# Performance work log

Hardware: AMD Instinct MI355X
Metric: run time of the kernel (lower is better)

Reference implementation:

```python
import jax, jax.numpy as jnp
import numpy as np

B, S, E, H = 2, 2048, 1024, 16
DH = E // H
SCALE = DH ** -0.5

def setup_inputs() -> dict:
    key = jax.random.key(0)
    ks = jax.random.split(key, 5)
    w_std = (2.0 / (E + E)) ** 0.5  # xavier-ish scale
    return {
        'x': jax.random.normal(ks[0], (B, S, E), jnp.float32),
        'Wq': jax.random.normal(ks[1], (E, E), jnp.float32) * w_std,
        'bq': jnp.zeros((E,), jnp.float32),
        'Wk': jax.random.normal(ks[2], (E, E), jnp.float32) * w_std,
        'bk': jnp.zeros((E,), jnp.float32),
        'Wv': jax.random.normal(ks[3], (E, E), jnp.float32) * w_std,
        'bv': jnp.zeros((E,), jnp.float32),
        'Wo': jax.random.normal(ks[4], (E, E), jnp.float32) * w_std,
        'bo': jnp.zeros((E,), jnp.float32),
    }

def reference(x, Wq, bq, Wk, bk, Wv, bv, Wo, bo):
    # self-attention: query = key = value = x; torch Linear: y = x @ W.T + b
    q = (x @ Wq.T + bq) * SCALE            # [B,S,E]
    k = x @ Wk.T + bk
    v = x @ Wv.T + bv
    # split heads -> [B,S,H,DH]
    q = q.reshape(B, S, H, DH)
    k = k.reshape(B, S, H, DH)
    v = v.reshape(B, S, H, DH)
    # explicit attention matrix [B,H,S,S] (faithful to unfused bmm path)
    scores = jnp.einsum('bqhd,bkhd->bhqk', q, k)
    probs = jax.nn.softmax(scores, axis=-1)
    attn = jnp.einsum('bhqk,bkhd->bqhd', probs, v).reshape(B, S, E)
    return attn @ Wo.T + bo                # [B,S,E]
```

## Files before the change

kernel.cpp:

```cpp
#include <hip/hip_runtime.h>
#include <stdint.h>

#define BB 2
#define SS 2048
#define EE 1024
#define HH 16
#define DHD 64
#define MM (BB*SS)
#define QSCALE (0.125f * 1.4426950408889634f)

typedef __bf16 bf16;
typedef __bf16 bf16x8 __attribute__((ext_vector_type(8)));
typedef __bf16 bf16x4 __attribute__((ext_vector_type(4)));
typedef float  f32x4  __attribute__((ext_vector_type(4)));
typedef unsigned short ushort8 __attribute__((ext_vector_type(8)));

#define MFMA16(a,b,c) __builtin_amdgcn_mfma_f32_16x16x32_bf16(a,b,c,0,0,0)

__device__ __forceinline__ void gload_lds16(const void* g, void* l) {
  __builtin_amdgcn_global_load_lds(
      (const __attribute__((address_space(1))) unsigned int*)g,
      (__attribute__((address_space(3))) unsigned int*)l, 16, 0, 0);
}

__device__ __forceinline__ unsigned short f2bf(float f) {
  union { float f; unsigned u; } v; v.f = f;
  return (unsigned short)((v.u + 0x7FFFu + ((v.u >> 16) & 1u)) >> 16);
}

__global__ void convert_kernel(const float* __restrict__ x,
                               const float* __restrict__ wq, const float* __restrict__ wk,
                               const float* __restrict__ wv, const float* __restrict__ wo,
                               unsigned short* __restrict__ xbf,
                               unsigned short* __restrict__ wqb, unsigned short* __restrict__ wkb,
                               unsigned short* __restrict__ wvb, unsigned short* __restrict__ wob) {
  long t = (long)blockIdx.x * blockDim.x + threadIdx.x;
  long base = t * 8;
  const float* src; unsigned short* dst; long off;
  if (base < 4194304L) { src = x; dst = xbf; off = base; }
  else {
    long r = base - 4194304L; int j = (int)(r >> 20); off = r & 1048575L;
    src = (j==0)?wq:(j==1)?wk:(j==2)?wv:wo;
    dst = (j==0)?wqb:(j==1)?wkb:(j==2)?wvb:wob;
  }
  const float4* s4 = (const float4*)(src + off);
  float4 a = s4[0], b = s4[1];
  ushort8 o;
  o[0]=f2bf(a.x); o[1]=f2bf(a.y); o[2]=f2bf(a.z); o[3]=f2bf(a.w);
  o[4]=f2bf(b.x); o[5]=f2bf(b.y); o[6]=f2bf(b.z); o[7]=f2bf(b.w);
  *(ushort8*)(dst + off) = o;
}

#define GS_STAGE(kbuf, kt) { \
    const size_t kb_ = (size_t)(kt) * 64; \
    char* d_ = lds + (kbuf) * 16384 + tid * 16; \
    gload_lds16(a0 + kb_, d_); \
    gload_lds16(a1 + kb_, d_ + 4096); \
    gload_lds16(b0 + kb_, d_ + 8192); \
    gload_lds16(b1 + kb_, d_ + 12288); \
  }

template<bool SWAP>
__device__ __forceinline__ void gemm_kloop(
    const char* a0, const char* a1, const char* b0, const char* b1,
    char* lds, const int tid, const int (&aoff)[4], const int (&boff)[4],
    f32x4 (&acc)[4][4]) {
  GS_STAGE(0, 0);
  GS_STAGE(1, 1);
  int cur = 0;
  for (int kt = 0; kt < 32; ++kt) {
    if (kt < 31) {
      asm volatile("s_waitcnt vmcnt(4)" ::: "memory");
    } else {
      asm volatile("s_waitcnt vmcnt(0)" ::: "memory");
    }
    __builtin_amdgcn_s_barrier();
    if (kt < 30) {
      int sb = cur + 2; if (sb >= 3) sb -= 3;
      GS_STAGE(sb, kt + 2);
    }
    const char* Ts = lds + cur * 16384;
    bf16x8 af[4], bfv[4];
#pragma unroll
    for (int mt=0; mt<4; ++mt) af[mt] = *(const bf16x8*)(Ts + aoff[mt]);
#pragma unroll
    for (int nt=0; nt<4; ++nt) bfv[nt] = *(const bf16x8*)(Ts + boff[nt]);
#pragma unroll
    for (int mt=0; mt<4; ++mt)
#pragma unroll
      for (int nt=0; nt<4; ++nt)
        acc[mt][nt] = SWAP ? MFMA16(bfv[nt], af[mt], acc[mt][nt])
                           : MFMA16(af[mt], bfv[nt], acc[mt][nt]);
    cur = (cur == 2) ? 0 : cur + 1;
  }
}

__global__ __launch_bounds__(256) void qkv_gemm(
    const bf16* __restrict__ xbf,
    const bf16* __restrict__ wqb, const bf16* __restrict__ wkb, const bf16* __restrict__ wvb,
    const float* __restrict__ bq, const float* __restrict__ bk, const float* __restrict__ bv,
    bf16* __restrict__ Q, bf16* __restrict__ K, bf16* __restrict__ VT) {
  __shared__ char lds[49152] __attribute__((aligned(16)));
  const int tid = threadIdx.x;
  const int bm = blockIdx.y * 128;
  const int bnG = blockIdx.x * 128;
  const int proj = bnG >> 10;
  const int bn = bnG & 1023;
  const bf16* wsel = (proj==0)?wqb:(proj==1)?wkb:wvb;
  const float* bias = (proj==0)?bq:(proj==1)?bk:bv;

  const int lane = tid & 63, w = tid >> 6;
  const int wm = (w>>1)*64, wn = (w&1)*64;
  const int c = lane & 15, g = lane >> 4;

  const int sr = tid >> 2;
  const int scb = ((tid & 3) * 16) ^ ((sr & 3) << 4);
  const char* a0 = (const char*)xbf  + ((size_t)(bm + sr     ) * 1024) * 2 + scb;
  const char* a1 = (const char*)xbf  + ((size_t)(bm + 64 + sr) * 1024) * 2 + scb;
  const char* b0 = (const char*)wsel + ((size_t)(bn + sr     ) * 1024) * 2 + scb;
  const char* b1 = (const char*)wsel + ((size_t)(bn + 64 + sr) * 1024) * 2 + scb;

  int aoff[4], boff[4];
#pragma unroll
  for (int mt=0; mt<4; ++mt) { int rr = wm + mt*16 + c; aoff[mt] = rr*64 + ((g*16) ^ ((rr&3)<<4)); }
#pragma unroll
  for (int nt=0; nt<4; ++nt) { int rr = wn + nt*16 + c; boff[nt] = 8192 + rr*64 + ((g*16) ^ ((rr&3)<<4)); }

  f32x4 acc[4][4];
#pragma unroll
  for (int mt=0; mt<4; ++mt)
#pragma unroll
    for (int nt=0; nt<4; ++nt) acc[mt][nt] = (f32x4){0.f,0.f,0.f,0.f};

  const int bidx = bm >> 11;
  const int srow = bm & 2047;

  if (proj != 2) {
    gemm_kloop<true>(a0, a1, b0, b1, lds, tid, aoff, boff, acc);
    bf16* dst = (proj == 0) ? Q : K;
    const float qs = (proj == 0) ? QSCALE : 1.0f;
#pragma unroll
    for (int nt=0; nt<4; ++nt) {
      const int n0 = bn + wn + nt*16 + g*4;
      const float4 b4 = *(const float4*)(bias + n0);
      const int h = n0 >> 6, d0 = n0 & 63;
#pragma unroll
      for (int mt=0; mt<4; ++mt) {
        const int s = srow + wm + mt*16 + c;
        bf16x4 pk;
        pk[0] = (bf16)((acc[mt][nt][0] + b4.x) * qs);
        pk[1] = (bf16)((acc[mt][nt][1] + b4.y) * qs);
        pk[2] = (bf16)((acc[mt][nt][2] + b4.z) * qs);
        pk[3] = (bf16)((acc[mt][nt][3] + b4.w) * qs);
        *(bf16x4*)(dst + (((size_t)(bidx*16 + h))*2048 + s)*64 + d0) = pk;
      }
    }
  } else {
    gemm_kloop<false>(a0, a1, b0, b1, lds, tid, aoff, boff, acc);
#pragma unroll
    for (int nt=0; nt<4; ++nt) {
      const int n = bn + wn + nt*16 + c;
      const float bv_ = bias[n];
      const int h = n >> 6, d = n & 63;
#pragma unroll
      for (int mt=0; mt<4; ++mt) {
        const int m0 = wm + mt*16 + g*4;
        bf16x4 pk;
#pragma unroll
        for (int r=0;r<4;++r) pk[r] = (bf16)(acc[mt][nt][r] + bv_);
        *(bf16x4*)(VT + (((size_t)(bidx*16 + h))*64 + d)*2048 + (srow + m0)) = pk;
      }
    }
  }
}

__global__ __launch_bounds__(256) void attn_kernel(
    const bf16* __restrict__ Q, const bf16* __restrict__ K,
    const bf16* __restrict__ VT, bf16* __restrict__ attn_out) {
  __shared__ char alds[32768] __attribute__((aligned(16)));
  const int tid = threadIdx.x;
  const int lane = tid & 63, w = tid >> 6;
  const int c = lane & 15, g = lane >> 4;
  const int x7 = c & 7;
  const int bh = blockIdx.y;
  const int qb = blockIdx.x * 64 + w * 16;
  const bf16* Qh = Q + (size_t)bh * 2048 * 64;
  const char* Khb = (const char*)(K  + (size_t)bh * 2048 * 64);
  const char* Vhb = (const char*)(VT + (size_t)bh * 64 * 2048);

  const int srow = tid >> 3, schunk = tid & 7;
  const int ssw = ((schunk ^ (srow & 7)) << 4);
  const char* srcK = Khb + (size_t)srow * 128  + ssw;
  const char* srcV = Vhb + (size_t)srow * 4096 + ssw;

#define ATT_STAGE(buf, kv) { \
    const char* sk_ = srcK + (size_t)(kv) * 128; \
    const char* sv_ = srcV + (size_t)(kv) * 2; \
    char* d_ = alds + (buf) * 16384 + tid * 16; \
    gload_lds16(sk_,            d_); \
    gload_lds16(sk_ + 32*128,   d_ + 4096); \
    gload_lds16(sv_,            d_ + 8192); \
    gload_lds16(sv_ + 32*4096,  d_ + 12288); \
  }

  bf16x8 qf0 = *(const bf16x8*)(Qh + (size_t)(qb + c)*64 + g*8);
  bf16x8 qf1 = *(const bf16x8*)(Qh + (size_t)(qb + c)*64 + 32 + g*8);

  f32x4 o[4];
#pragma unroll
  for (int dt=0; dt<4; ++dt) o[dt] = (f32x4){0.f,0.f,0.f,0.f};
  float m = -1e30f, l = 0.f;

  ATT_STAGE(0, 0);
  asm volatile("s_waitcnt vmcnt(0)" ::: "memory");
  __builtin_amdgcn_s_barrier();

  for (int t = 0; t < 32; ++t) {
    const int cur = t & 1;
    if (t < 31) ATT_STAGE(cur ^ 1, (t + 1) * 64);

    const char* Kl = alds + cur * 16384;
    const char* Vl = Kl + 8192;

    f32x4 st[4];
#pragma unroll
    for (int ks = 0; ks < 4; ++ks) {
      const char* kr = Kl + (ks*16 + c) * 128;
      bf16x8 k0 = *(const bf16x8*)(kr + (((g    ) ^ x7) << 4));
      bf16x8 k1 = *(const bf16x8*)(kr + (((g + 4) ^ x7) << 4));
      f32x4 z = (f32x4){0.f,0.f,0.f,0.f};
      z = MFMA16(k0, qf0, z);
      z = MFMA16(k1, qf1, z);
      st[ks] = z;
    }

    float tmax = -1e30f;
#pragma unroll
    for (int ks = 0; ks < 4; ++ks)
      tmax = fmaxf(tmax, fmaxf(fmaxf(st[ks][0], st[ks][1]), fmaxf(st[ks][2], st[ks][3])));
    tmax = fmaxf(tmax, __shfl_xor(tmax, 16, 64));
    tmax = fmaxf(tmax, __shfl_xor(tmax, 32, 64));
    if (!__all(tmax <= m + 8.f)) {
      const float mnew = fmaxf(m, tmax);
      const float corr = __builtin_exp2f(m - mnew);
      l *= corr;
#pragma unroll
      for (int dt=0; dt<4; ++dt) o[dt] *= corr;
      m = mnew;
    }
    float p[4][4]; float ps = 0.f;
#pragma unroll
    for (int ks = 0; ks < 4; ++ks)
#pragma unroll
      for (int r = 0; r < 4; ++r) { p[ks][r] = __builtin_exp2f(st[ks][r] - m); ps += p[ks][r]; }
    ps += __shfl_xor(ps, 16, 64);
    ps += __shfl_xor(ps, 32, 64);
    l += ps;

    bf16x8 pfA, pfB;
#pragma unroll
    for (int r = 0; r < 4; ++r) {
      pfA[r] = (bf16)p[0][r]; pfA[4+r] = (bf16)p[1][r];
      pfB[r] = (bf16)p[2][r]; pfB[4+r] = (bf16)p[3][r];
    }

#pragma unroll
    for (int dt = 0; dt < 4; ++dt) {
      const char* vr = Vl + (dt*16 + c) * 128;
      const int i8 = (g & 1) * 8, gh = g >> 1;
      bf16x4 va0 = *(const bf16x4*)(vr + (((gh    ) ^ x7) << 4) + i8);
      bf16x4 va1 = *(const bf16x4*)(vr + (((gh + 2) ^ x7) << 4) + i8);
      bf16x4 vb0 = *(const bf16x4*)(vr + (((gh + 4) ^ x7) << 4) + i8);
      bf16x4 vb1 = *(const bf16x4*)(vr + (((gh + 6) ^ x7) << 4) + i8);
      bf16x8 vfA = __builtin_shufflevector(va0, va1, 0,1,2,3,4,5,6,7);
      bf16x8 vfB = __builtin_shufflevector(vb0, vb1, 0,1,2,3,4,5,6,7);
      o[dt] = MFMA16(vfA, pfA, o[dt]);
      o[dt] = MFMA16(vfB, pfB, o[dt]);
    }

    if (t < 31) {
      asm volatile("s_waitcnt vmcnt(0)" ::: "memory");
      __builtin_amdgcn_s_barrier();
    }
  }
#undef ATT_STAGE

  const float inv = 1.0f / l;
  const int srow_q = qb + c;
  const int b = bh >> 4, h = bh & 15;
  bf16* outrow = attn_out + ((size_t)(b*2048 + srow_q))*1024 + h*64;
#pragma unroll
  for (int dt=0; dt<4; ++dt) {
    bf16x4 ov;
#pragma unroll
    for (int r=0;r<4;++r) ov[r] = (bf16)(o[dt][r] * inv);
    *(bf16x4*)(outrow + dt*16 + g*4) = ov;
  }
}

__global__ __launch_bounds__(256) void out_gemm(
    const bf16* __restrict__ A, const bf16* __restrict__ W,
    const float* __restrict__ bias, float* __restrict__ out) {
  __shared__ char lds[36864] __attribute__((aligned(16)));
  const int tid = threadIdx.x;
  const int bm = blockIdx.y * 64, bn = blockIdx.x * 128;
  const int lane = tid & 63, w = tid >> 6;
  const int c = lane & 15, g = lane >> 4;

  const int sr = tid >> 2;
  const int scb = ((tid & 3) * 16) ^ ((sr & 3) << 4);
  const char* a0 = (const char*)A + ((size_t)(bm + sr     ) * 1024) * 2 + scb;
  const char* b0 = (const char*)W + ((size_t)(bn + sr     ) * 1024) * 2 + scb;
  const char* b1 = (const char*)W + ((size_t)(bn + 64 + sr) * 1024) * 2 + scb;

#define OUT_STAGE(kbuf, kt) { \
    const size_t kb_ = (size_t)(kt) * 64; \
    char* d_ = lds + (kbuf) * 12288 + tid * 16; \
    gload_lds16(a0 + kb_, d_); \
    gload_lds16(b0 + kb_, d_ + 4096); \
    gload_lds16(b1 + kb_, d_ + 8192); \
  }

  int aoff[4], boff[2];
#pragma unroll
  for (int mt=0; mt<4; ++mt) { int rr = mt*16 + c; aoff[mt] = rr*64 + ((g*16) ^ ((rr&3)<<4)); }
#pragma unroll
  for (int nt=0; nt<2; ++nt) { int rr = w*32 + nt*16 + c; boff[nt] = 4096 + rr*64 + ((g*16) ^ ((rr&3)<<4)); }

  f32x4 acc[4][2];
#pragma unroll
  for (int mt=0; mt<4; ++mt)
#pragma unroll
    for (int nt=0; nt<2; ++nt) acc[mt][nt] = (f32x4){0.f,0.f,0.f,0.f};

  OUT_STAGE(0, 0);
  OUT_STAGE(1, 1);
  int cur = 0;
  for (int kt = 0; kt < 32; ++kt) {
    if (kt < 31) {
      asm volatile("s_waitcnt vmcnt(3)" ::: "memory");
    } else {
      asm volatile("s_waitcnt vmcnt(0)" ::: "memory");
    }
    __builtin_amdgcn_s_barrier();
    if (kt < 30) {
      int sb = cur + 2; if (sb >= 3) sb -= 3;
      OUT_STAGE(sb, kt + 2);
    }
    const char* Ts = lds + cur * 12288;
    bf16x8 af[4], bfv[2];
#pragma unroll
    for (int mt=0; mt<4; ++mt) af[mt] = *(const bf16x8*)(Ts + aoff[mt]);
#pragma unroll
    for (int nt=0; nt<2; ++nt) bfv[nt] = *(const bf16x8*)(Ts + boff[nt]);
#pragma unroll
    for (int mt=0; mt<4; ++mt)
#pragma unroll
      for (int nt=0; nt<2; ++nt)
        acc[mt][nt] = MFMA16(bfv[nt], af[mt], acc[mt][nt]);
    cur = (cur == 2) ? 0 : cur + 1;
  }
#undef OUT_STAGE

#pragma unroll
  for (int nt=0; nt<2; ++nt) {
    const int n0 = bn + w*32 + nt*16 + g*4;
    const float4 b4 = *(const float4*)(bias + n0);
#pragma unroll
    for (int mt=0; mt<4; ++mt) {
      const int m0 = bm + mt*16 + c;
      float4 ov;
      ov.x = acc[mt][nt][0] + b4.x;
      ov.y = acc[mt][nt][1] + b4.y;
      ov.z = acc[mt][nt][2] + b4.z;
      ov.w = acc[mt][nt][3] + b4.w;
      *(float4*)(out + (size_t)m0*1024 + n0) = ov;
    }
  }
}

extern "C" void kernel_launch(void* const* d_in, const int* in_sizes, int n_in,
                              void* d_out, int out_size, void* d_ws, size_t ws_size,
                              hipStream_t stream) {
  const float* x  = (const float*)d_in[0];
  const float* Wq = (const float*)d_in[1];
  const float* bq = (const float*)d_in[2];
  const float* Wk = (const float*)d_in[3];
  const float* bk = (const float*)d_in[4];
  const float* Wv = (const float*)d_in[5];
  const float* bv = (const float*)d_in[6];
  const float* Wo = (const float*)d_in[7];
  const float* bo = (const float*)d_in[8];

  char* ws = (char*)d_ws;
  const size_t MiB = 1u << 20;
  unsigned short* xbf = (unsigned short*)(ws);
  unsigned short* wqb = (unsigned short*)(ws +  8*MiB);
  unsigned short* wkb = (unsigned short*)(ws + 10*MiB);
  unsigned short* wvb = (unsigned short*)(ws + 12*MiB);
  unsigned short* wob = (unsigned short*)(ws + 14*MiB);
  bf16* Qb    = (bf16*)(ws + 16*MiB);
  bf16* Kb    = (bf16*)(ws + 24*MiB);
  bf16* VTb   = (bf16*)(ws + 32*MiB);
  bf16* attnb = (bf16*)(ws + 40*MiB);

  convert_kernel<<<4096, 256, 0, stream>>>(x, Wq, Wk, Wv, Wo, xbf, wqb, wkb, wvb, wob);
  qkv_gemm<<<dim3(24, 32), 256, 0, stream>>>(
      (const bf16*)xbf, (const bf16*)wqb, (const bf16*)wkb, (const bf16*)wvb,
      bq, bk, bv, Qb, Kb, VTb);
  attn_kernel<<<dim3(32, 32), 256, 0, stream>>>(Qb, Kb, VTb, attnb);
  out_gemm<<<dim3(8, 64), 256, 0, stream>>>(attnb, (const bf16*)wob, bo, (float*)d_out);
}
```

Measured before the change: 224.8 us.

## Switch attention to 32x32x16 MFMA with 512-thread blocks of 256 queries

Rewrites the attention inner loop to use 32x32x16 bf16 MFMA tiles, so each wave handles 32 query rows and the P matrix is repacked through cross-half lane shuffles instead of 16x16 fragments. Blocks grow to 8 waves covering 256 queries, which shares each staged K/V tile across more queries and cuts the number of LDS staging loads per thread. The larger tile reduces LDS reads and reduction shuffles per FLOP, but it uses more registers per lane for the 16-wide accumulators. It also launches only 256 blocks, which may leave compute units underused.

```diff
diff --git a/kernel.cpp b/kernel.cpp
--- a/kernel.cpp
+++ b/kernel.cpp
@@ -12,10 +12,13 @@
 typedef __bf16 bf16;
 typedef __bf16 bf16x8 __attribute__((ext_vector_type(8)));
 typedef __bf16 bf16x4 __attribute__((ext_vector_type(4)));
+typedef __bf16 bf16x2 __attribute__((ext_vector_type(2)));
 typedef float  f32x4  __attribute__((ext_vector_type(4)));
+typedef float  f32x16 __attribute__((ext_vector_type(16)));
 typedef unsigned short ushort8 __attribute__((ext_vector_type(8)));
 
 #define MFMA16(a,b,c) __builtin_amdgcn_mfma_f32_16x16x32_bf16(a,b,c,0,0,0)
+#define MFMA32(a,b,c) __builtin_amdgcn_mfma_f32_32x32x16_bf16(a,b,c,0,0,0)
 
 __device__ __forceinline__ void gload_lds16(const void* g, void* l) {
   __builtin_amdgcn_global_load_lds(
@@ -174,41 +177,37 @@
   }
 }
 
-__global__ __launch_bounds__(256) void attn_kernel(
+__global__ __launch_bounds__(512) void attn_kernel(
     const bf16* __restrict__ Q, const bf16* __restrict__ K,
     const bf16* __restrict__ VT, bf16* __restrict__ attn_out) {
   __shared__ char alds[32768] __attribute__((aligned(16)));
   const int tid = threadIdx.x;
-  const int lane = tid & 63, w = tid >> 6;
-  const int c = lane & 15, g = lane >> 4;
-  const int x7 = c & 7;
+  const int L = tid & 63, wid = tid >> 6;
+  const int q5 = L & 31, h = L >> 5;
   const int bh = blockIdx.y;
-  const int qb = blockIdx.x * 64 + w * 16;
+  const int qbase = blockIdx.x * 256;
   const bf16* Qh = Q + (size_t)bh * 2048 * 64;
   const char* Khb = (const char*)(K  + (size_t)bh * 2048 * 64);
   const char* Vhb = (const char*)(VT + (size_t)bh * 64 * 2048);
 
-  const int srow = tid >> 3, schunk = tid & 7;
-  const int ssw = ((schunk ^ (srow & 7)) << 4);
+  const int srow = tid >> 3, sch = tid & 7;
+  const int ssw = ((sch ^ (srow & 7)) << 4);
   const char* srcK = Khb + (size_t)srow * 128  + ssw;
   const char* srcV = Vhb + (size_t)srow * 4096 + ssw;
 
 #define ATT_STAGE(buf, kv) { \
-    const char* sk_ = srcK + (size_t)(kv) * 128; \
-    const char* sv_ = srcV + (size_t)(kv) * 2; \
-    char* d_ = alds + (buf) * 16384 + tid * 16; \
-    gload_lds16(sk_,            d_); \
-    gload_lds16(sk_ + 32*128,   d_ + 4096); \
-    gload_lds16(sv_,            d_ + 8192); \
-    gload_lds16(sv_ + 32*4096,  d_ + 12288); \
-  }
-
-  bf16x8 qf0 = *(const bf16x8*)(Qh + (size_t)(qb + c)*64 + g*8);
-  bf16x8 qf1 = *(const bf16x8*)(Qh + (size_t)(qb + c)*64 + 32 + g*8);
-
-  f32x4 o[4];
-#pragma unroll
-  for (int dt=0; dt<4; ++dt) o[dt] = (f32x4){0.f,0.f,0.f,0.f};
+    gload_lds16(srcK + (size_t)(kv) * 128, alds + (buf) * 16384 + tid * 16); \
+    gload_lds16(srcV + (size_t)(kv) * 2,   alds + (buf) * 16384 + 8192 + tid * 16); \
+  }
+
+  const int qrow = qbase + wid * 32 + q5;
+  bf16x8 qf[4];
+#pragma unroll
+  for (int dk = 0; dk < 4; ++dk)
+    qf[dk] = *(const bf16x8*)(Qh + (size_t)qrow * 64 + dk * 16 + h * 8);
+
+  f32x16 o0 = {0,0,0,0,0,0,0,0,0,0,0,0,0,0,0,0};
+  f32x16 o1 = {0,0,0,0,0,0,0,0,0,0,0,0,0,0,0,0};
   float m = -1e30f, l = 0.f;
 
   ATT_STAGE(0, 0);
@@ -222,60 +221,88 @@
     const char* Kl = alds + cur * 16384;
     const char* Vl = Kl + 8192;
 
-    f32x4 st[4];
-#pragma unroll
-    for (int ks = 0; ks < 4; ++ks) {
-      const char* kr = Kl + (ks*16 + c) * 128;
-      bf16x8 k0 = *(const bf16x8*)(kr + (((g    ) ^ x7) << 4));
-      bf16x8 k1 = *(const bf16x8*)(kr + (((g + 4) ^ x7) << 4));
-      f32x4 z = (f32x4){0.f,0.f,0.f,0.f};
-      z = MFMA16(k0, qf0, z);
-      z = MFMA16(k1, qf1, z);
-      st[ks] = z;
+    f32x16 st0 = {0,0,0,0,0,0,0,0,0,0,0,0,0,0,0,0};
+    f32x16 st1 = {0,0,0,0,0,0,0,0,0,0,0,0,0,0,0,0};
+#pragma unroll
+    for (int dk = 0; dk < 4; ++dk) {
+      const int r0 = q5;
+      bf16x8 k0 = *(const bf16x8*)(Kl + r0*128        + (((2*dk + h) ^ (r0 & 7)) << 4));
+      const int r1 = 32 + q5;
+      bf16x8 k1 = *(const bf16x8*)(Kl + r1*128        + (((2*dk + h) ^ (r1 & 7)) << 4));
+      st0 = MFMA32(k0, qf[dk], st0);
+      st1 = MFMA32(k1, qf[dk], st1);
     }
 
     float tmax = -1e30f;
 #pragma unroll
-    for (int ks = 0; ks < 4; ++ks)
-      tmax = fmaxf(tmax, fmaxf(fmaxf(st[ks][0], st[ks][1]), fmaxf(st[ks][2], st[ks][3])));
-    tmax = fmaxf(tmax, __shfl_xor(tmax, 16, 64));
+    for (int r = 0; r < 16; ++r) { tmax = fmaxf(tmax, st0[r]); tmax = fmaxf(tmax, st1[r]); }
     tmax = fmaxf(tmax, __shfl_xor(tmax, 32, 64));
     if (!__all(tmax <= m + 8.f)) {
       const float mnew = fmaxf(m, tmax);
       const float corr = __builtin_exp2f(m - mnew);
       l *= corr;
-#pragma unroll
-      for (int dt=0; dt<4; ++dt) o[dt] *= corr;
+      o0 *= corr; o1 *= corr;
       m = mnew;
     }
-    float p[4][4]; float ps = 0.f;
-#pragma unroll
-    for (int ks = 0; ks < 4; ++ks)
-#pragma unroll
-      for (int r = 0; r < 4; ++r) { p[ks][r] = __builtin_exp2f(st[ks][r] - m); ps += p[ks][r]; }
-    ps += __shfl_xor(ps, 16, 64);
+
+    unsigned pk0[4][2], pk1[4][2];
+    float ps = 0.f;
+#pragma unroll
+    for (int j = 0; j < 4; ++j)
+#pragma unroll
+      for (int a = 0; a < 2; ++a) {
+        {
+          float x0 = __builtin_exp2f(st0[4*j+2*a]     - m);
+          float x1 = __builtin_exp2f(st0[4*j+2*a + 1] - m);
+          ps += x0 + x1;
+          union { bf16x2 v; unsigned u; } z; z.v[0] = (bf16)x0; z.v[1] = (bf16)x1;
+          pk0[j][a] = z.u;
+        }
+        {
+          float x0 = __builtin_exp2f(st1[4*j+2*a]     - m);
+          float x1 = __builtin_exp2f(st1[4*j+2*a + 1] - m);
+          ps += x0 + x1;
+          union { bf16x2 v; unsigned u; } z; z.v[0] = (bf16)x0; z.v[1] = (bf16)x1;
+          pk1[j][a] = z.u;
+        }
+      }
     ps += __shfl_xor(ps, 32, 64);
     l += ps;
 
-    bf16x8 pfA, pfB;
-#pragma unroll
-    for (int r = 0; r < 4; ++r) {
-      pfA[r] = (bf16)p[0][r]; pfA[4+r] = (bf16)p[1][r];
-      pfB[r] = (bf16)p[2][r]; pfB[4+r] = (bf16)p[3][r];
-    }
-
-#pragma unroll
-    for (int dt = 0; dt < 4; ++dt) {
-      const char* vr = Vl + (dt*16 + c) * 128;
-      const int i8 = (g & 1) * 8, gh = g >> 1;
-      bf16x4 va0 = *(const bf16x4*)(vr + (((gh    ) ^ x7) << 4) + i8);
-      bf16x4 va1 = *(const bf16x4*)(vr + (((gh + 2) ^ x7) << 4) + i8);
-      bf16x4 vb0 = *(const bf16x4*)(vr + (((gh + 4) ^ x7) << 4) + i8);
-      bf16x4 vb1 = *(const bf16x4*)(vr + (((gh + 6) ^ x7) << 4) + i8);
-      bf16x8 vfA = __builtin_shufflevector(va0, va1, 0,1,2,3,4,5,6,7);
-      bf16x8 vfB = __builtin_shufflevector(vb0, vb1, 0,1,2,3,4,5,6,7);
-      o[dt] = MFMA16(vfA, pfA, o[dt]);
-      o[dt] = MFMA16(vfB, pfB, o[dt]);
+    bf16x8 pf[4];
+#pragma unroll
+    for (int c = 0; c < 4; ++c) {
+      const int cl = c & 1;
+      unsigned own0, own1, snd0, snd1;
+      if (c < 2) {
+        own0 = h ? pk0[2*cl+1][0] : pk0[2*cl][0];
+        own1 = h ? pk0[2*cl+1][1] : pk0[2*cl][1];
+        snd0 = h ? pk0[2*cl][0]   : pk0[2*cl+1][0];
+        snd1 = h ? pk0[2*cl][1]   : pk0[2*cl+1][1];
+      } else {
+        own0 = h ? pk1[2*cl+1][0] : pk1[2*cl][0];
+        own1 = h ? pk1[2*cl+1][1] : pk1[2*cl][1];
+        snd0 = h ? pk1[2*cl][0]   : pk1[2*cl+1][0];
+        snd1 = h ? pk1[2*cl][1]   : pk1[2*cl+1][1];
+      }
+      unsigned sx0 = (unsigned)__shfl_xor((int)snd0, 32, 64);
+      unsigned sx1 = (unsigned)__shfl_xor((int)snd1, 32, 64);
+      union { unsigned u[4]; bf16x8 v; } fr;
+      fr.u[0] = h ? sx0 : own0;
+      fr.u[1] = h ? sx1 : own1;
+      fr.u[2] = h ? own0 : sx0;
+      fr.u[3] = h ? own1 : sx1;
+      pf[c] = fr.v;
+    }
+
+#pragma unroll
+    for (int c = 0; c < 4; ++c) {
+      const int r0 = q5;
+      bf16x8 v0 = *(const bf16x8*)(Vl + r0*128        + (((2*c + h) ^ (r0 & 7)) << 4));
+      const int r1 = 32 + q5;
+      bf16x8 v1 = *(const bf16x8*)(Vl + r1*128        + (((2*c + h) ^ (r1 & 7)) << 4));
+      o0 = MFMA32(v0, pf[c], o0);
+      o1 = MFMA32(v1, pf[c], o1);
     }
 
     if (t < 31) {
@@ -286,15 +313,17 @@
 #undef ATT_STAGE
 
   const float inv = 1.0f / l;
-  const int srow_q = qb + c;
-  const int b = bh >> 4, h = bh & 15;
-  bf16* outrow = attn_out + ((size_t)(b*2048 + srow_q))*1024 + h*64;
-#pragma unroll
-  for (int dt=0; dt<4; ++dt) {
+  const int b = bh >> 4, hh = bh & 15;
+  bf16* outrow = attn_out + ((size_t)(b*2048 + qrow))*1024 + hh*64;
+#pragma unroll
+  for (int j = 0; j < 4; ++j) {
     bf16x4 ov;
 #pragma unroll
-    for (int r=0;r<4;++r) ov[r] = (bf16)(o[dt][r] * inv);
-    *(bf16x4*)(outrow + dt*16 + g*4) = ov;
+    for (int i = 0; i < 4; ++i) ov[i] = (bf16)(o0[4*j+i] * inv);
+    *(bf16x4*)(outrow + 8*j + 4*h) = ov;
+#pragma unroll
+    for (int i = 0; i < 4; ++i) ov[i] = (bf16)(o1[4*j+i] * inv);
+    *(bf16x4*)(outrow + 32 + 8*j + 4*h) = ov;
   }
 }
 
@@ -408,6 +437,6 @@
   qkv_gemm<<<dim3(24, 32), 256, 0, stream>>>(
       (const bf16*)xbf, (const bf16*)wqb, (const bf16*)wkb, (const bf16*)wvb,
       bq, bk, bv, Qb, Kb, VTb);
-  attn_kernel<<<dim3(32, 32), 256, 0, stream>>>(Qb, Kb, VTb, attnb);
+  attn_kernel<<<dim3(8, 32), 512, 0, stream>>>(Qb, Kb, VTb, attnb);
   out_gemm<<<dim3(8, 64), 256, 0, stream>>>(attnb, (const bf16*)wob, bo, (float*)d_out);
 }
```

After: 203.4 us. 9.5% less time.
